# Optimization experiments

Measured on AMD Instinct MI355X. Metric: run time of the kernel, lower is better.

The kernel has to match this reference:

```python
import jax, jax.numpy as jnp
import numpy as np

B = 64          # batch
NV = 6890       # SMPL vertices
NF = 13776      # SMPL faces
NHD = 20000     # HD (uniformly resampled) vertices
NP = 24         # SMPL parts
COP_W = 10.0
COP_K = 100.0
EPS = 1e-6


def setup_inputs() -> dict:
    key = jax.random.key(0)
    k1, k2, k3, k4, k5 = jax.random.split(key, 5)
    vertices = jax.random.normal(k1, (B, NV, 3), jnp.float32)
    hd_operator = jax.random.uniform(k2, (NHD, NV), jnp.float32) / NV
    faces = jax.random.randint(k3, (NF, 3), 0, NV)          # triangle vertex ids
    vert_fid = jax.random.randint(k4, (NHD,), 0, NF)        # HD vert -> source face
    face_part = jax.random.randint(k5, (NF,), 0, NP)        # face -> body part
    return {"vertices": vertices, "hd_operator": hd_operator,
            "faces": faces, "vert_fid": vert_fid, "face_part": face_part}


def reference(vertices, hd_operator, faces, vert_fid, face_part):
    # --- per-part volume: signed tetrahedron volume per face, summed per part ---
    tri = vertices[:, faces]                      # [B, NF, 3, 3]
    v0, v1, v2 = tri[:, :, 0], tri[:, :, 1], tri[:, :, 2]
    vol_f = jnp.abs(jnp.einsum('bfi,bfi->bf', v0, jnp.cross(v1, v2))) / 6.0  # [B, NF]
    part_onehot = jax.nn.one_hot(face_part, NP, dtype=vol_f.dtype)           # [NF, NP]
    per_part_volume = jnp.einsum('bf,fp->bp', vol_f, part_onehot)            # [B, NP]

    vertices_hd = jnp.einsum('nm,bmd->bnd', hd_operator, vertices)           # [B, NHD, 3]

    # --- map each HD vertex to the volume of its part ---
    part_of_vert = face_part[vert_fid]                                       # [NHD]
    vol_vert = per_part_volume[:, part_of_vert][..., None]                   # [B, NHD, 1]

    # --- volume-weighted COM ---
    com = jnp.sum(vertices_hd * vol_vert, axis=1) / jnp.sum(vol_vert, axis=1)  # [B, 3]

    # --- pressure-weighted COP ---
    h = vertices_hd[:, :, 1]  # vertex height above ground plane (y)
    pw = jnp.where(h < 0.0, 1.0 - COP_K * h, jnp.exp(-COP_W * h))            # [B, NHD]
    cop = jnp.sum(vertices_hd * pw[..., None], axis=1) / (
        jnp.sum(pw, axis=1, keepdims=True) + EPS)                            # [B, 3]

    # --- stability loss: xz distance between COM and COP ---
    d = com - cop
    return jnp.sqrt(d[:, 0] ** 2 + d[:, 2] ** 2)                             # [B]
```

## Files before the change

kernel.cpp:

```cpp
#include <hip/hip_runtime.h>
#include <cstdint>

#define B_    64
#define NV_   6890
#define NF_   13776
#define NHD_  20000
#define NP_   24
#define NCH   216
#define KSPL  4
#define CPW   54

#define OFF_PPV   0u
#define OFF_RED   6144u
#define ZERO_BYTES 7680u
#define OFF_VC    7680u

typedef __attribute__((ext_vector_type(8))) __bf16 bf16x8;
typedef __attribute__((ext_vector_type(8))) unsigned short u16x8;
typedef __attribute__((ext_vector_type(4))) float f32x4;

__device__ __forceinline__ unsigned short f2bf(float f) {
    unsigned u = __float_as_uint(f);
    u = (u + 0x7fffu + ((u >> 16) & 1u)) >> 16;
    return (unsigned short)u;
}

__global__ __launch_bounds__(256) void k0v_pack(const float* __restrict__ verts,
                                                unsigned short* __restrict__ Vc) {
    int idx = blockIdx.x * 256 + threadIdx.x;
    int j    = idx & 7;
    int lane = (idx >> 3) & 63;
    int ct   = idx >> 9;
    int t    = ct % 12;
    int c    = ct / 12;
    int lm   = lane & 15;
    int kk   = (lane >> 4) * 8 + j;
    int bd   = t * 16 + lm;
    int d    = bd >> 6, b = bd & 63;
    int k    = c * 32 + kk;
    float v  = (k < NV_) ? verts[((size_t)b * NV_ + k) * 3 + d] : 0.f;
    Vc[idx] = f2bf(v);
}

__global__ __launch_bounds__(256) void k1_vol(const float* __restrict__ verts,
                                              const int* __restrict__ faces,
                                              const int* __restrict__ face_part,
                                              float* __restrict__ ppv) {
    __shared__ float bins[NP_];
    int b = blockIdx.y;
    int f = blockIdx.x * 256 + threadIdx.x;
    if (threadIdx.x < NP_) bins[threadIdx.x] = 0.f;
    __syncthreads();
    if (f < NF_) {
        int i0 = faces[3 * f], i1 = faces[3 * f + 1], i2 = faces[3 * f + 2];
        const float* vb = verts + (size_t)b * NV_ * 3;
        float ax = vb[3 * i0], ay = vb[3 * i0 + 1], az = vb[3 * i0 + 2];
        float bx = vb[3 * i1], by = vb[3 * i1 + 1], bz = vb[3 * i1 + 2];
        float cx = vb[3 * i2], cy = vb[3 * i2 + 1], cz = vb[3 * i2 + 2];
        float crx = by * cz - bz * cy;
        float cry = bz * cx - bx * cz;
        float crz = bx * cy - by * cx;
        float vol = fabsf(ax * crx + ay * cry + az * crz) * (1.0f / 6.0f);
        atomicAdd(&bins[face_part[f]], vol);
    }
    __syncthreads();
    if (threadIdx.x < NP_) atomicAdd(&ppv[b * NP_ + threadIdx.x], bins[threadIdx.x]);
}

#define ACCP 193
__global__ __launch_bounds__(256) void kf_fused(const float* __restrict__ Hm,
                                                const unsigned short* __restrict__ Vc,
                                                const int* __restrict__ vert_fid,
                                                const int* __restrict__ face_part,
                                                const float* __restrict__ ppv,
                                                float* __restrict__ red) {
    __shared__ float accs[32 * ACCP];
    __shared__ float reds[B_ * 6];
    const int tid  = threadIdx.x;
    const int lane = tid & 63;
    const int s    = tid >> 6;
    const int lm   = lane & 15;
    const int kg   = lane >> 4;
    const int n0   = blockIdx.x * 32;
    const float* Arow0 = Hm + (size_t)(n0 + lm) * NV_;
    const float* Arow1 = Hm + (size_t)(n0 + 16 + lm) * NV_;
    const int cs = s * CPW, ce = cs + CPW;
    const int ce_main = (s == KSPL - 1) ? (NCH - 1) : ce;

    f32x4 acc0[12], acc1[12];
#pragma unroll
    for (int t = 0; t < 12; ++t) {
        acc0[t] = (f32x4){0.f, 0.f, 0.f, 0.f};
        acc1[t] = (f32x4){0.f, 0.f, 0.f, 0.f};
    }

    float2 a[4], b[4];
    {
        int k0 = cs * 32 + kg * 8;
#pragma unroll
        for (int j = 0; j < 4; ++j) {
            a[j] = *reinterpret_cast<const float2*>(Arow0 + k0 + 2 * j);
            b[j] = *reinterpret_cast<const float2*>(Arow1 + k0 + 2 * j);
        }
    }

#pragma unroll 1
    for (int c = cs; c < ce_main; ++c) {
        const u16x8* Bp = reinterpret_cast<const u16x8*>(Vc) + (size_t)c * 768 + lane;
        u16x8 Bu[12];
#pragma unroll
        for (int t = 0; t < 12; ++t) Bu[t] = Bp[t * 64];
        __builtin_amdgcn_sched_barrier(0);

        const int cpf = (c + 1 < ce_main) ? (c + 1) : cs;
        const int k0n = cpf * 32 + kg * 8;
        float2 na[4], nb[4];
#pragma unroll
        for (int j = 0; j < 4; ++j) {
            na[j] = *reinterpret_cast<const float2*>(Arow0 + k0n + 2 * j);
            nb[j] = *reinterpret_cast<const float2*>(Arow1 + k0n + 2 * j);
        }
        __builtin_amdgcn_sched_barrier(0);

        bf16x8 Af0, Af1;
#pragma unroll
        for (int j = 0; j < 4; ++j) {
            Af0[2 * j]     = (__bf16)a[j].x;
            Af0[2 * j + 1] = (__bf16)a[j].y;
            Af1[2 * j]     = (__bf16)b[j].x;
            Af1[2 * j + 1] = (__bf16)b[j].y;
        }
#pragma unroll
        for (int t = 0; t < 12; ++t)
            acc0[t] = __builtin_amdgcn_mfma_f32_16x16x32_bf16(
                Af0, __builtin_bit_cast(bf16x8, Bu[t]), acc0[t], 0, 0, 0);
#pragma unroll
        for (int t = 0; t < 12; ++t)
            acc1[t] = __builtin_amdgcn_mfma_f32_16x16x32_bf16(
                Af1, __builtin_bit_cast(bf16x8, Bu[t]), acc1[t], 0, 0, 0);
#pragma unroll
        for (int j = 0; j < 4; ++j) { a[j] = na[j]; b[j] = nb[j]; }
    }

    if (ce > ce_main) {
        const int c = NCH - 1;
        const u16x8* Bp = reinterpret_cast<const u16x8*>(Vc) + (size_t)c * 768 + lane;
        u16x8 Bu[12];
#pragma unroll
        for (int t = 0; t < 12; ++t) Bu[t] = Bp[t * 64];
        const int k0 = c * 32 + kg * 8;
        bf16x8 Af0, Af1;
#pragma unroll
        for (int j = 0; j < 8; ++j) {
            int k = k0 + j;
            float fa = (k < NV_) ? Arow0[k] : 0.f;
            float fb = (k < NV_) ? Arow1[k] : 0.f;
            Af0[j] = (__bf16)fa;
            Af1[j] = (__bf16)fb;
        }
#pragma unroll
        for (int t = 0; t < 12; ++t)
            acc0[t] = __builtin_amdgcn_mfma_f32_16x16x32_bf16(
                Af0, __builtin_bit_cast(bf16x8, Bu[t]), acc0[t], 0, 0, 0);
#pragma unroll
        for (int t = 0; t < 12; ++t)
            acc1[t] = __builtin_amdgcn_mfma_f32_16x16x32_bf16(
                Af1, __builtin_bit_cast(bf16x8, Bu[t]), acc1[t], 0, 0, 0);
    }

    for (int i = tid; i < 32 * ACCP; i += 256) accs[i] = 0.f;
    for (int i = tid; i < B_ * 6; i += 256) reds[i] = 0.f;
    __syncthreads();
#pragma unroll
    for (int t = 0; t < 12; ++t)
#pragma unroll
        for (int r = 0; r < 4; ++r) {
            atomicAdd(&accs[(kg * 4 + r) * ACCP + t * 16 + lm], acc0[t][r]);
            atomicAdd(&accs[(16 + kg * 4 + r) * ACCP + t * 16 + lm], acc1[t][r]);
        }
    __syncthreads();

    {
        int bb = tid & 63;
        int r0 = tid >> 6;
        float scx = 0.f, scz = 0.f, smx = 0.f, smz = 0.f, ssp = 0.f, ssw = 0.f;
#pragma unroll
        for (int q = 0; q < 8; ++q) {
            int row = q * 4 + r0;
            int n = n0 + row;
            float x = accs[row * ACCP + bb];
            float h = accs[row * ACCP + 64 + bb];
            float z = accs[row * ACCP + 128 + bb];
            float pwv = (h < 0.f) ? (1.f - 100.f * h) : expf(-10.f * h);
            int part = face_part[vert_fid[n]];
            float w = ppv[bb * NP_ + part];
            scx += pwv * x; scz += pwv * z;
            smx += w * x;   smz += w * z;
            ssp += pwv;     ssw += w;
        }
        atomicAdd(&reds[bb * 6 + 0], scx);
        atomicAdd(&reds[bb * 6 + 1], scz);
        atomicAdd(&reds[bb * 6 + 2], smx);
        atomicAdd(&reds[bb * 6 + 3], smz);
        atomicAdd(&reds[bb * 6 + 4], ssp);
        atomicAdd(&reds[bb * 6 + 5], ssw);
    }
    __syncthreads();
    for (int i = tid; i < B_ * 6; i += 256) atomicAdd(&red[i], reds[i]);
}

__global__ __launch_bounds__(64) void k5_final(const float* __restrict__ red,
                                               float* __restrict__ out) {
    int b = threadIdx.x;
    if (b < B_) {
        float sp   = red[b * 6 + 4] + 1e-6f;
        float sw   = red[b * 6 + 5];
        float copx = red[b * 6 + 0] / sp;
        float copz = red[b * 6 + 1] / sp;
        float comx = red[b * 6 + 2] / sw;
        float comz = red[b * 6 + 3] / sw;
        float dx = comx - copx, dz = comz - copz;
        out[b] = sqrtf(dx * dx + dz * dz);
    }
}

extern "C" void kernel_launch(void* const* d_in, const int* in_sizes, int n_in,
                              void* d_out, int out_size, void* d_ws, size_t ws_size,
                              hipStream_t stream) {
    const float* verts     = (const float*)d_in[0];
    const float* Hm        = (const float*)d_in[1];
    const int*   faces     = (const int*)d_in[2];
    const int*   vert_fid  = (const int*)d_in[3];
    const int*   face_part = (const int*)d_in[4];
    char* ws = (char*)d_ws;
    float*          ppv = (float*)(ws + OFF_PPV);
    float*          red = (float*)(ws + OFF_RED);
    unsigned short* Vc  = (unsigned short*)(ws + OFF_VC);
    float* out = (float*)d_out;

    hipMemsetAsync(d_ws, 0, ZERO_BYTES, stream);
    hipLaunchKernelGGL(k0v_pack, dim3((NCH * 12 * 512) / 256), dim3(256), 0, stream, verts, Vc);
    hipLaunchKernelGGL(k1_vol, dim3(54, 64), dim3(256), 0, stream, verts, faces, face_part, ppv);
    hipLaunchKernelGGL(kf_fused, dim3(NHD_ / 32), dim3(256), 0, stream,
                       Hm, Vc, vert_fid, face_part, ppv, red);
    hipLaunchKernelGGL(k5_final, dim3(1), dim3(64), 0, stream, red, out);
}
```

Measured before the change: 310.0 us.

## Use single-wave blocks with double-buffered LDS staging of packed vertices

Each fused block now has one 64-thread wave that walks the full K range instead of four waves splitting it. The B operand (packed bf16 vertices) is staged asynchronously into a double-buffered LDS region with global_load_lds, so loads overlap the MFMAs. The LDS atomic cross-wave reduction is gone: the epilogue works on MFMA accumulators in registers and reduces with shuffles before global atomics. The memset is replaced with a tiny init kernel. The trade-off is fewer waves per block and less K-parallelism per block, which may reduce latency hiding, and every chunk waits on vmcnt(0).

```diff
diff --git a/kernel.cpp b/kernel.cpp
--- a/kernel.cpp
+++ b/kernel.cpp
@@ -7,22 +7,23 @@
 #define NHD_  20000
 #define NP_   24
 #define NCH   216
-#define KSPL  4
-#define CPW   54
+#define BUF_HW 6144
 
 #define OFF_PPV   0u
 #define OFF_RED   6144u
-#define ZERO_BYTES 7680u
 #define OFF_VC    7680u
 
 typedef __attribute__((ext_vector_type(8))) __bf16 bf16x8;
-typedef __attribute__((ext_vector_type(8))) unsigned short u16x8;
 typedef __attribute__((ext_vector_type(4))) float f32x4;
 
 __device__ __forceinline__ unsigned short f2bf(float f) {
     unsigned u = __float_as_uint(f);
     u = (u + 0x7fffu + ((u >> 16) & 1u)) >> 16;
     return (unsigned short)u;
+}
+
+__global__ __launch_bounds__(256) void k_init(float* __restrict__ z) {
+    for (int i = threadIdx.x; i < 1920; i += 256) z[i] = 0.f;
 }
 
 __global__ __launch_bounds__(256) void k0v_pack(const float* __restrict__ verts,
@@ -67,25 +68,19 @@
     if (threadIdx.x < NP_) atomicAdd(&ppv[b * NP_ + threadIdx.x], bins[threadIdx.x]);
 }
 
-#define ACCP 193
-__global__ __launch_bounds__(256) void kf_fused(const float* __restrict__ Hm,
-                                                const unsigned short* __restrict__ Vc,
-                                                const int* __restrict__ vert_fid,
-                                                const int* __restrict__ face_part,
-                                                const float* __restrict__ ppv,
-                                                float* __restrict__ red) {
-    __shared__ float accs[32 * ACCP];
-    __shared__ float reds[B_ * 6];
-    const int tid  = threadIdx.x;
-    const int lane = tid & 63;
-    const int s    = tid >> 6;
+__global__ __launch_bounds__(64) void kf_fused(const float* __restrict__ Hm,
+                                               const unsigned short* __restrict__ Vc,
+                                               const int* __restrict__ vert_fid,
+                                               const int* __restrict__ face_part,
+                                               const float* __restrict__ ppv,
+                                               float* __restrict__ red) {
+    __shared__ unsigned short Vl[2 * BUF_HW];
+    const int lane = threadIdx.x;
     const int lm   = lane & 15;
     const int kg   = lane >> 4;
     const int n0   = blockIdx.x * 32;
     const float* Arow0 = Hm + (size_t)(n0 + lm) * NV_;
     const float* Arow1 = Hm + (size_t)(n0 + 16 + lm) * NV_;
-    const int cs = s * CPW, ce = cs + CPW;
-    const int ce_main = (s == KSPL - 1) ? (NCH - 1) : ce;
 
     f32x4 acc0[12], acc1[12];
 #pragma unroll
@@ -94,34 +89,32 @@
         acc1[t] = (f32x4){0.f, 0.f, 0.f, 0.f};
     }
 
+    auto stage = [&](int cc, unsigned short* dst) {
+        const unsigned short* src = Vc + (size_t)cc * BUF_HW + lane * 8;
+#pragma unroll
+        for (int i = 0; i < 12; ++i)
+            __builtin_amdgcn_global_load_lds(
+                (const __attribute__((address_space(1))) void*)(src + i * 512),
+                (__attribute__((address_space(3))) void*)(dst + i * 512), 16, 0, 0);
+    };
+    auto loadA = [&](int cc, float2* ra, float2* rb) {
+        int k0 = cc * 32 + kg * 8;
+#pragma unroll
+        for (int j = 0; j < 4; ++j) {
+            ra[j] = *reinterpret_cast<const float2*>(Arow0 + k0 + 2 * j);
+            rb[j] = *reinterpret_cast<const float2*>(Arow1 + k0 + 2 * j);
+        }
+    };
+
+    stage(0, &Vl[0]);
     float2 a[4], b[4];
-    {
-        int k0 = cs * 32 + kg * 8;
-#pragma unroll
-        for (int j = 0; j < 4; ++j) {
-            a[j] = *reinterpret_cast<const float2*>(Arow0 + k0 + 2 * j);
-            b[j] = *reinterpret_cast<const float2*>(Arow1 + k0 + 2 * j);
-        }
-    }
-
+    loadA(0, a, b);
+
+    int p = 0;
 #pragma unroll 1
-    for (int c = cs; c < ce_main; ++c) {
-        const u16x8* Bp = reinterpret_cast<const u16x8*>(Vc) + (size_t)c * 768 + lane;
-        u16x8 Bu[12];
-#pragma unroll
-        for (int t = 0; t < 12; ++t) Bu[t] = Bp[t * 64];
-        __builtin_amdgcn_sched_barrier(0);
-
-        const int cpf = (c + 1 < ce_main) ? (c + 1) : cs;
-        const int k0n = cpf * 32 + kg * 8;
-        float2 na[4], nb[4];
-#pragma unroll
-        for (int j = 0; j < 4; ++j) {
-            na[j] = *reinterpret_cast<const float2*>(Arow0 + k0n + 2 * j);
-            nb[j] = *reinterpret_cast<const float2*>(Arow1 + k0n + 2 * j);
-        }
-        __builtin_amdgcn_sched_barrier(0);
-
+    for (int c = 0; c < NCH - 1; ++c) {
+        asm volatile("s_waitcnt vmcnt(0)" ::: "memory");
+        __builtin_amdgcn_sched_barrier(0);
         bf16x8 Af0, Af1;
 #pragma unroll
         for (int j = 0; j < 4; ++j) {
@@ -130,25 +123,34 @@
             Af1[2 * j]     = (__bf16)b[j].x;
             Af1[2 * j + 1] = (__bf16)b[j].y;
         }
-#pragma unroll
-        for (int t = 0; t < 12; ++t)
-            acc0[t] = __builtin_amdgcn_mfma_f32_16x16x32_bf16(
-                Af0, __builtin_bit_cast(bf16x8, Bu[t]), acc0[t], 0, 0, 0);
-#pragma unroll
-        for (int t = 0; t < 12; ++t)
-            acc1[t] = __builtin_amdgcn_mfma_f32_16x16x32_bf16(
-                Af1, __builtin_bit_cast(bf16x8, Bu[t]), acc1[t], 0, 0, 0);
-#pragma unroll
-        for (int j = 0; j < 4; ++j) { a[j] = na[j]; b[j] = nb[j]; }
-    }
-
-    if (ce > ce_main) {
-        const int c = NCH - 1;
-        const u16x8* Bp = reinterpret_cast<const u16x8*>(Vc) + (size_t)c * 768 + lane;
-        u16x8 Bu[12];
-#pragma unroll
-        for (int t = 0; t < 12; ++t) Bu[t] = Bp[t * 64];
-        const int k0 = c * 32 + kg * 8;
+        __builtin_amdgcn_sched_barrier(0);
+        stage(c + 1, &Vl[(p ^ 1) * BUF_HW]);
+        int cpf = (c + 1 < NCH - 1) ? (c + 1) : (NCH - 2);
+        loadA(cpf, a, b);
+        __builtin_amdgcn_sched_barrier(0);
+        bf16x8 Bu[12];
+        const unsigned short* bp = &Vl[p * BUF_HW] + lane * 8;
+#pragma unroll
+        for (int t = 0; t < 12; ++t)
+            Bu[t] = *reinterpret_cast<const bf16x8*>(bp + t * 512);
+#pragma unroll
+        for (int t = 0; t < 12; ++t)
+            acc0[t] = __builtin_amdgcn_mfma_f32_16x16x32_bf16(Af0, Bu[t], acc0[t], 0, 0, 0);
+#pragma unroll
+        for (int t = 0; t < 12; ++t)
+            acc1[t] = __builtin_amdgcn_mfma_f32_16x16x32_bf16(Af1, Bu[t], acc1[t], 0, 0, 0);
+        p ^= 1;
+    }
+
+    {
+        asm volatile("s_waitcnt vmcnt(0)" ::: "memory");
+        __builtin_amdgcn_sched_barrier(0);
+        bf16x8 Bu[12];
+        const unsigned short* bp = &Vl[p * BUF_HW] + lane * 8;
+#pragma unroll
+        for (int t = 0; t < 12; ++t)
+            Bu[t] = *reinterpret_cast<const bf16x8*>(bp + t * 512);
+        int k0 = (NCH - 1) * 32 + kg * 8;
         bf16x8 Af0, Af1;
 #pragma unroll
         for (int j = 0; j < 8; ++j) {
@@ -160,53 +162,65 @@
         }
 #pragma unroll
         for (int t = 0; t < 12; ++t)
-            acc0[t] = __builtin_amdgcn_mfma_f32_16x16x32_bf16(
-                Af0, __builtin_bit_cast(bf16x8, Bu[t]), acc0[t], 0, 0, 0);
-#pragma unroll
-        for (int t = 0; t < 12; ++t)
-            acc1[t] = __builtin_amdgcn_mfma_f32_16x16x32_bf16(
-                Af1, __builtin_bit_cast(bf16x8, Bu[t]), acc1[t], 0, 0, 0);
-    }
-
-    for (int i = tid; i < 32 * ACCP; i += 256) accs[i] = 0.f;
-    for (int i = tid; i < B_ * 6; i += 256) reds[i] = 0.f;
-    __syncthreads();
-#pragma unroll
-    for (int t = 0; t < 12; ++t)
+            acc0[t] = __builtin_amdgcn_mfma_f32_16x16x32_bf16(Af0, Bu[t], acc0[t], 0, 0, 0);
+#pragma unroll
+        for (int t = 0; t < 12; ++t)
+            acc1[t] = __builtin_amdgcn_mfma_f32_16x16x32_bf16(Af1, Bu[t], acc1[t], 0, 0, 0);
+    }
+
+    int part0[4], part1[4];
+#pragma unroll
+    for (int r = 0; r < 4; ++r) {
+        part0[r] = face_part[vert_fid[n0 + kg * 4 + r]];
+        part1[r] = face_part[vert_fid[n0 + 16 + kg * 4 + r]];
+    }
+    float sums[4][6];
+#pragma unroll
+    for (int t = 0; t < 4; ++t)
+#pragma unroll
+        for (int q = 0; q < 6; ++q) sums[t][q] = 0.f;
+
+#pragma unroll
+    for (int t = 0; t < 4; ++t) {
+        int bcol = t * 16 + lm;
 #pragma unroll
         for (int r = 0; r < 4; ++r) {
-            atomicAdd(&accs[(kg * 4 + r) * ACCP + t * 16 + lm], acc0[t][r]);
-            atomicAdd(&accs[(16 + kg * 4 + r) * ACCP + t * 16 + lm], acc1[t][r]);
-        }
-    __syncthreads();
-
-    {
-        int bb = tid & 63;
-        int r0 = tid >> 6;
-        float scx = 0.f, scz = 0.f, smx = 0.f, smz = 0.f, ssp = 0.f, ssw = 0.f;
-#pragma unroll
-        for (int q = 0; q < 8; ++q) {
-            int row = q * 4 + r0;
-            int n = n0 + row;
-            float x = accs[row * ACCP + bb];
-            float h = accs[row * ACCP + 64 + bb];
-            float z = accs[row * ACCP + 128 + bb];
-            float pwv = (h < 0.f) ? (1.f - 100.f * h) : expf(-10.f * h);
-            int part = face_part[vert_fid[n]];
-            float w = ppv[bb * NP_ + part];
-            scx += pwv * x; scz += pwv * z;
-            smx += w * x;   smz += w * z;
-            ssp += pwv;     ssw += w;
-        }
-        atomicAdd(&reds[bb * 6 + 0], scx);
-        atomicAdd(&reds[bb * 6 + 1], scz);
-        atomicAdd(&reds[bb * 6 + 2], smx);
-        atomicAdd(&reds[bb * 6 + 3], smz);
-        atomicAdd(&reds[bb * 6 + 4], ssp);
-        atomicAdd(&reds[bb * 6 + 5], ssw);
-    }
-    __syncthreads();
-    for (int i = tid; i < B_ * 6; i += 256) atomicAdd(&red[i], reds[i]);
+            {
+                float x = acc0[t][r], h = acc0[4 + t][r], z = acc0[8 + t][r];
+                float pwv = (h < 0.f) ? (1.f - 100.f * h) : expf(-10.f * h);
+                float w = ppv[bcol * NP_ + part0[r]];
+                sums[t][0] += pwv * x; sums[t][1] += pwv * z;
+                sums[t][2] += w * x;   sums[t][3] += w * z;
+                sums[t][4] += pwv;     sums[t][5] += w;
+            }
+            {
+                float x = acc1[t][r], h = acc1[4 + t][r], z = acc1[8 + t][r];
+                float pwv = (h < 0.f) ? (1.f - 100.f * h) : expf(-10.f * h);
+                float w = ppv[bcol * NP_ + part1[r]];
+                sums[t][0] += pwv * x; sums[t][1] += pwv * z;
+                sums[t][2] += w * x;   sums[t][3] += w * z;
+                sums[t][4] += pwv;     sums[t][5] += w;
+            }
+        }
+    }
+#pragma unroll
+    for (int t = 0; t < 4; ++t)
+#pragma unroll
+        for (int q = 0; q < 6; ++q) {
+            float v = sums[t][q];
+            v += __shfl_xor(v, 16);
+            v += __shfl_xor(v, 32);
+            sums[t][q] = v;
+        }
+    if (kg == 0) {
+#pragma unroll
+        for (int t = 0; t < 4; ++t) {
+            int bcol = t * 16 + lm;
+#pragma unroll
+            for (int q = 0; q < 6; ++q)
+                atomicAdd(&red[bcol * 6 + q], sums[t][q]);
+        }
+    }
 }
 
 __global__ __launch_bounds__(64) void k5_final(const float* __restrict__ red,
@@ -238,10 +252,10 @@
     unsigned short* Vc  = (unsigned short*)(ws + OFF_VC);
     float* out = (float*)d_out;
 
-    hipMemsetAsync(d_ws, 0, ZERO_BYTES, stream);
+    hipLaunchKernelGGL(k_init, dim3(1), dim3(256), 0, stream, (float*)ws);
     hipLaunchKernelGGL(k0v_pack, dim3((NCH * 12 * 512) / 256), dim3(256), 0, stream, verts, Vc);
     hipLaunchKernelGGL(k1_vol, dim3(54, 64), dim3(256), 0, stream, verts, faces, face_part, ppv);
-    hipLaunchKernelGGL(kf_fused, dim3(NHD_ / 32), dim3(256), 0, stream,
+    hipLaunchKernelGGL(kf_fused, dim3(NHD_ / 32), dim3(64), 0, stream,
                        Hm, Vc, vert_fid, face_part, ppv, red);
     hipLaunchKernelGGL(k5_final, dim3(1), dim3(64), 0, stream, red, out);
 }
```

Result: slower. 361.1 us (+16.5%).
